# Optimization experiments

Measured on AMD Instinct MI355X. Metric: run time of the kernel, lower is better.

The kernel has to match this reference:

```python
import jax, jax.numpy as jnp
import numpy as np
import math

L = 6; D = 768; NH = 12; DH = D // NH; V = 2048; CTX = 512; B = 16; T = 512
PAD_ID = 0; PAD_X = 18; PAD_Y = 32; N_ACTIONS = 9


def _layernorm(x, s, b, eps=1e-5):
    m = jnp.mean(x, axis=-1, keepdims=True)
    v = jnp.mean((x - m) ** 2, axis=-1, keepdims=True)
    return (x - m) * jax.lax.rsqrt(v + eps) * s + b


def setup_inputs() -> dict:
    key = jax.random.key(0)
    ks = jax.random.split(key, 16)
    s = 0.02
    x_emb = jax.random.normal(ks[4], (19, D), jnp.float32) * s
    x_emb = x_emb.at[PAD_X].set(0.0)  # padding_idx row is zero in torch
    y_emb = jax.random.normal(ks[5], (33, D), jnp.float32) * s
    y_emb = y_emb.at[PAD_Y].set(0.0)
    return {
        "history_cards": jax.random.randint(ks[0], (B, T), 0, V),
        "history_players": jax.random.randint(ks[1], (B, T), 0, 2),
        "deck": jax.random.randint(ks[2], (B, 8), 0, V),
        "opp_deck": jax.random.randint(ks[3], (B, 8), 0, V),
        "tok_emb": jax.random.normal(ks[6], (V, D), jnp.float32) * s,
        "player_emb": jax.random.normal(ks[7], (2, D), jnp.float32) * s,
        "pos_emb": jax.random.normal(ks[8], (CTX, D), jnp.float32) * s,
        "x_emb": x_emb,
        "y_emb": y_emb,
        "ln1_s": jnp.ones((L, D), jnp.float32),
        "ln1_b": jnp.zeros((L, D), jnp.float32),
        "qkv_w": jax.random.normal(ks[9], (L, D, 3 * D), jnp.float32) * s,
        "qkv_b": jnp.zeros((L, 3 * D), jnp.float32),
        "proj_w": jax.random.normal(ks[10], (L, D, D), jnp.float32) * s,
        "proj_b": jnp.zeros((L, D), jnp.float32),
        "ln2_s": jnp.ones((L, D), jnp.float32),
        "ln2_b": jnp.zeros((L, D), jnp.float32),
        "fc1_w": jax.random.normal(ks[11], (L, D, 4 * D), jnp.float32) * s,
        "fc1_b": jnp.zeros((L, 4 * D), jnp.float32),
        "fc2_w": jax.random.normal(ks[12], (L, 4 * D, D), jnp.float32) * s,
        "fc2_b": jnp.zeros((L, D), jnp.float32),
        "lnf_s": jnp.ones((D,), jnp.float32),
        "lnf_b": jnp.zeros((D,), jnp.float32),
        "head_w": jax.random.normal(ks[13], (D, N_ACTIONS), jnp.float32) * s,
        "head_b": jnp.zeros((N_ACTIONS,), jnp.float32),
    }


def reference(history_cards, history_players, deck, opp_deck,
              tok_emb, player_emb, pos_emb, x_emb, y_emb,
              ln1_s, ln1_b, qkv_w, qkv_b, proj_w, proj_b,
              ln2_s, ln2_b, fc1_w, fc1_b, fc2_w, fc2_b,
              lnf_s, lnf_b, head_w, head_b):
    Bc, Tc = history_cards.shape
    attn_mask = history_cards != PAD_ID                      # (B,T) True = valid
    all_pad = ~jnp.any(attn_mask, axis=1)
    attn_mask = attn_mask.at[:, 0].set(attn_mask[:, 0] | all_pad)

    # multi-embedding sum (history_x/history_y are None => padding rows = 0)
    h = (tok_emb[history_cards]
         + player_emb[jnp.clip(history_players, 0, 1)]
         + x_emb[PAD_X] + y_emb[PAD_Y]
         + jnp.mean(tok_emb[deck], axis=1, keepdims=True)
         + jnp.mean(tok_emb[opp_deck], axis=1, keepdims=True))
    x = h + pos_emb[:Tc][None]                               # (B,T,D)

    causal = jnp.tril(jnp.ones((Tc, Tc), bool))
    mask = causal[None, None, :, :] & attn_mask[:, None, None, :]  # (B,1,T,T)
    neg_inf = jnp.float32(-jnp.inf)
    scale = 1.0 / math.sqrt(DH)

    for i in range(L):
        # attention
        xn = _layernorm(x, ln1_s[i], ln1_b[i])
        qkv = xn @ qkv_w[i] + qkv_b[i]
        q, k, v = jnp.split(qkv, 3, axis=-1)
        q = q.reshape(Bc, Tc, NH, DH)
        k = k.reshape(Bc, Tc, NH, DH)
        v = v.reshape(Bc, Tc, NH, DH)
        scores = jnp.einsum('bihd,bjhd->bhij', q, k) * scale
        scores = jnp.where(mask, scores, neg_inf)
        w = jax.nn.softmax(scores, axis=-1)
        w = jnp.nan_to_num(w, nan=0.0, posinf=0.0, neginf=0.0)
        y = jnp.einsum('bhij,bjhd->bihd', w, v).reshape(Bc, Tc, D)
        x = x + (y @ proj_w[i] + proj_b[i])
        # MLP
        xn = _layernorm(x, ln2_s[i], ln2_b[i])
        hmid = jax.nn.gelu(xn @ fc1_w[i] + fc1_b[i], approximate=False)
        x = x + (hmid @ fc2_w[i] + fc2_b[i])

    x = _layernorm(x, lnf_s, lnf_b)
    last_idx = jnp.clip(jnp.sum(attn_mask.astype(jnp.int32), axis=1) - 1, 0, None)
    last_h = x[jnp.arange(Bc), last_idx]                     # (B,D)
    return last_h @ head_w + head_b                          # (B,9)
```

## Files before the change

kernel.cpp:

```cpp
#include <hip/hip_runtime.h>
#include <hip/hip_bf16.h>
#include <math.h>

typedef __hip_bfloat16 bf16;
typedef __bf16 bf16x8 __attribute__((ext_vector_type(8)));
typedef float f32x4 __attribute__((ext_vector_type(4)));

__device__ __forceinline__ float b2f(bf16 v){ return __bfloat162float(v); }
__device__ __forceinline__ bf16  f2b(float v){ return __float2bfloat16(v); }

__device__ __forceinline__ float gelu_f(float v){
    float y = v * (1.f + 0.044715f * v * v);
    return v / (1.f + __expf(-1.5957691216057308f * y));
}

__device__ __forceinline__ void gl_lds16(const bf16* g, bf16* l) {
    __builtin_amdgcn_global_load_lds((const __attribute__((address_space(1))) unsigned int*)g,
                                     (__attribute__((address_space(3))) unsigned int*)l, 16, 0, 0);
}

__device__ __forceinline__ uint2 pack4bf(const float* v){
    union { unsigned short e[4]; uint2 u; } pk;
    #pragma unroll
    for (int r = 0; r < 4; r++) pk.e[r] = __builtin_bit_cast(unsigned short, f2b(v[r]));
    return pk.u;
}

__device__ __forceinline__ void phase_bar() {
    __builtin_amdgcn_sched_barrier(0);
    __builtin_amdgcn_s_barrier();
    __builtin_amdgcn_sched_barrier(0);
}

__global__ __launch_bounds__(256) void deckmean_k(const int* __restrict__ deck, const int* __restrict__ opp,
                                                  const float* __restrict__ tok, float* __restrict__ deckm)
{
    int b = blockIdx.x, w = blockIdx.y;
    const int* dk = (w ? opp : deck) + b * 8;
    int idx[8];
    #pragma unroll
    for (int j = 0; j < 8; j++) idx[j] = dk[j];
    float* out = deckm + (size_t)(w * 16 + b) * 768;
    for (int d = threadIdx.x; d < 768; d += 256) {
        float s = 0.f;
        #pragma unroll
        for (int j = 0; j < 8; j++) s += tok[(size_t)idx[j] * 768 + d];
        out[d] = s * 0.125f;
    }
}

__global__ __launch_bounds__(512) void mask_k(const int* __restrict__ cards, int* __restrict__ maskb,
                                              int* __restrict__ lastidx)
{
    int b = blockIdx.x, t = threadIdx.x;
    int m = (cards[b * 512 + t] != 0) ? 1 : 0;
    maskb[b * 512 + t] = m;
    __shared__ int red[512];
    red[t] = m; __syncthreads();
    for (int st = 256; st > 0; st >>= 1) { if (t < st) red[t] += red[t + st]; __syncthreads(); }
    if (t == 0) {
        int cnt = red[0];
        if (cnt == 0) { maskb[b * 512] = 1; cnt = 1; }
        lastidx[b] = cnt - 1;
    }
}

__global__ __launch_bounds__(256) void embed_k(const int* __restrict__ cards, const int* __restrict__ players,
                                               const float* __restrict__ tok, const float* __restrict__ pemb,
                                               const float* __restrict__ pos, const float* __restrict__ deckm,
                                               float* __restrict__ x)
{
    int t = blockIdx.x;
    int b = t >> 9, ti = t & 511;
    int cd = cards[t];
    int p = players[t]; p = p < 0 ? 0 : (p > 1 ? 1 : p);
    const float* tr  = tok  + (size_t)cd * 768;
    const float* pr  = pemb + (size_t)p  * 768;
    const float* po  = pos  + (size_t)ti * 768;
    const float* dm = deckm + (size_t)b * 768;
    const float* om = deckm + (size_t)(16 + b) * 768;
    float* xr = x + (size_t)t * 768;
    for (int d = threadIdx.x; d < 768; d += 256)
        xr[d] = tr[d] + pr[d] + po[d] + dm[d] + om[d];
}

__global__ __launch_bounds__(192) void ln_k(const float* __restrict__ x, const float* __restrict__ s,
                                            const float* __restrict__ b, bf16* __restrict__ out)
{
    int row = blockIdx.x, tid = threadIdx.x;
    float4 v = ((const float4*)(x + (size_t)row * 768))[tid];
    float sum = v.x + v.y + v.z + v.w;
    float sq  = v.x * v.x + v.y * v.y + v.z * v.z + v.w * v.w;
    #pragma unroll
    for (int off = 32; off > 0; off >>= 1) {
        sum += __shfl_xor(sum, off, 64);
        sq  += __shfl_xor(sq,  off, 64);
    }
    __shared__ float red[6];
    int wv = tid >> 6;
    if ((tid & 63) == 0) { red[wv] = sum; red[3 + wv] = sq; }
    __syncthreads();
    float S = red[0] + red[1] + red[2];
    float Q = red[3] + red[4] + red[5];
    float mean = S * (1.f / 768.f);
    float var  = Q * (1.f / 768.f) - mean * mean;
    float rstd = rsqrtf(var + 1e-5f);
    float4 sv = ((const float4*)s)[tid];
    float4 bv = ((const float4*)b)[tid];
    float o[4] = { (v.x - mean) * rstd * sv.x + bv.x, (v.y - mean) * rstd * sv.y + bv.y,
                   (v.z - mean) * rstd * sv.z + bv.z, (v.w - mean) * rstd * sv.w + bv.w };
    ((uint2*)(out + (size_t)row * 768))[tid] = pack4bf(o);
}

__global__ __launch_bounds__(256) void transpose4_k(const float* __restrict__ qw, const float* __restrict__ pw,
                                                    const float* __restrict__ f1, const float* __restrict__ f2,
                                                    bf16* __restrict__ oq, bf16* __restrict__ op,
                                                    bf16* __restrict__ o1, bf16* __restrict__ o2)
{
    int t = blockIdx.x;
    const float* in; bf16* out; int K, N, nbx;
    if (t < 432)       { in = qw; out = oq; K = 768;  N = 2304; nbx = 36; }
    else if (t < 576)  { in = pw; out = op; K = 768;  N = 768;  t -= 432;  nbx = 12; }
    else if (t < 1152) { in = f1; out = o1; K = 768;  N = 3072; t -= 576;  nbx = 48; }
    else               { in = f2; out = o2; K = 3072; N = 768;  t -= 1152; nbx = 12; }
    int n0 = (t % nbx) * 64, k0 = (t / nbx) * 64;
    int kq = threadIdx.x & 15, nq = threadIdx.x >> 4;
    float4 rr[4];
    #pragma unroll
    for (int r = 0; r < 4; r++)
        rr[r] = *(const float4*)&in[(size_t)(k0 + kq * 4 + r) * N + n0 + nq * 4];
    const float* fp = (const float*)rr;
    #pragma unroll
    for (int c = 0; c < 4; c++) {
        float v[4] = { fp[c], fp[4 + c], fp[8 + c], fp[12 + c] };
        *(uint2*)&out[(size_t)(n0 + nq * 4 + c) * K + k0 + kq * 4] = pack4bf(v);
    }
}

__global__ __launch_bounds__(512, 2) void gemm256_k(const bf16* __restrict__ A, const bf16* __restrict__ BT,
                                                    const float* __restrict__ bias, bf16* __restrict__ out,
                                                    int N, int K, int act, int nbn)
{
    __shared__ __align__(16) bf16 Asb[2][256 * 64];
    __shared__ __align__(16) bf16 Bsb[2][256 * 64];

    const int tid  = threadIdx.x;
    const int lane = tid & 63, wid = tid >> 6;
    const int quad = lane >> 4, l16 = lane & 15;
    const int wr = wid >> 2, wc = wid & 3;
    const int xr  = l16 & 7;
    const int cg0 = quad ^ xr;
    const int cg1 = cg0 ^ 4;

    const int nwg  = gridDim.x;
    const int wgid = ((int)blockIdx.x & 7) * (nwg >> 3) + ((int)blockIdx.x >> 3);
    const int mt = wgid / nbn, nt = wgid - mt * nbn;
    const int m0 = mt * 256, n0 = nt * 256;

    const int srow = wid * 8 + (lane >> 3);
    const int scg  = (lane & 7) ^ (lane >> 3);
    const bf16* sa[4]; const bf16* sb[4];
    #pragma unroll
    for (int s = 0; s < 4; s++) {
        sa[s] = A  + (size_t)(m0 + s * 64 + srow) * K + scg * 8;
        sb[s] = BT + (size_t)(n0 + s * 64 + srow) * K + scg * 8;
    }

#define STG_A(s, b) gl_lds16(sa[s], &Asb[b][((s) * 64 + wid * 8) * 64])
#define STG_B(s, b) gl_lds16(sb[s], &Bsb[b][((s) * 64 + wid * 8) * 64])
#define LD_B(cg) { _Pragma("unroll") for (int ni = 0; ni < 4; ni++) \
    bfv[ni] = __builtin_bit_cast(bf16x8, *(const uint4*)&Bc[(wc * 64 + ni * 16 + l16) * 64 + (cg) * 8]); }
#define LD_A(rb, cg) { _Pragma("unroll") for (int mi = 0; mi < 4; mi++) \
    afv[mi] = __builtin_bit_cast(bf16x8, *(const uint4*)&Ac[(wr * 128 + (rb) + mi * 16 + l16) * 64 + (cg) * 8]); }
#define MFMA16(MB) { _Pragma("unroll") for (int mi = 0; mi < 4; mi++) \
    _Pragma("unroll") for (int ni = 0; ni < 4; ni++) \
        acc[(MB) + mi][ni] = __builtin_amdgcn_mfma_f32_16x16x32_bf16(bfv[ni], afv[mi], acc[(MB) + mi][ni], 0, 0, 0); }

    STG_A(0, 0); STG_A(2, 0);
    STG_B(0, 0); STG_B(1, 0); STG_B(2, 0); STG_B(3, 0);
    STG_A(1, 0); STG_A(3, 0);
    #pragma unroll
    for (int s = 0; s < 4; s++) { sa[s] += 64; sb[s] += 64; }

    f32x4 acc[8][4] = {};

    asm volatile("s_waitcnt vmcnt(2)" ::: "memory");
    phase_bar();

    const int NKT = K >> 6;
    for (int kt = 0; kt < NKT; kt++) {
        const bf16* Ac = Asb[kt & 1];
        const bf16* Bc = Bsb[kt & 1];
        const int nxt = (kt & 1) ^ 1;
        const bool pf = (kt + 1 < NKT);
        bf16x8 bfv[4], afv[4];

        LD_B(cg0); LD_A(0, cg0);
        if (pf) {
            STG_A(0, nxt); STG_A(2, nxt);
            STG_B(0, nxt); STG_B(1, nxt); STG_B(2, nxt); STG_B(3, nxt);
            asm volatile("s_waitcnt vmcnt(6)" ::: "memory");
        } else {
            asm volatile("s_waitcnt vmcnt(0)" ::: "memory");
        }
        phase_bar();
        __builtin_amdgcn_s_setprio(1); MFMA16(0); __builtin_amdgcn_s_setprio(0);
        phase_bar();

        LD_A(64, cg0);
        if (pf) { STG_A(1, nxt); STG_A(3, nxt); }
        phase_bar();
        __builtin_amdgcn_s_setprio(1); MFMA16(4); __builtin_amdgcn_s_setprio(0);
        phase_bar();

        LD_B(cg1); LD_A(0, cg1);
        phase_bar();
        __builtin_amdgcn_s_setprio(1); MFMA16(0); __builtin_amdgcn_s_setprio(0);
        phase_bar();

        LD_A(64, cg1);
        phase_bar();
        __builtin_amdgcn_s_setprio(1); MFMA16(4); __builtin_amdgcn_s_setprio(0);
        asm volatile("s_waitcnt vmcnt(2)" ::: "memory");
        phase_bar();

        #pragma unroll
        for (int s = 0; s < 4; s++) { sa[s] += 64; sb[s] += 64; }
    }

    float4 bv[4];
    #pragma unroll
    for (int ni = 0; ni < 4; ni++)
        bv[ni] = *(const float4*)&bias[n0 + wc * 64 + ni * 16 + quad * 4];

    #pragma unroll
    for (int mi = 0; mi < 8; mi++) {
        const int m = m0 + wr * 128 + mi * 16 + l16;
        #pragma unroll
        for (int ni = 0; ni < 4; ni++) {
            const int nb2 = n0 + wc * 64 + ni * 16 + quad * 4;
            float v[4] = { acc[mi][ni][0] + bv[ni].x, acc[mi][ni][1] + bv[ni].y,
                           acc[mi][ni][2] + bv[ni].z, acc[mi][ni][3] + bv[ni].w };
            if (act) {
                #pragma unroll
                for (int r = 0; r < 4; r++) v[r] = gelu_f(v[r]);
            }
            *(uint2*)&out[(size_t)m * N + nb2] = pack4bf(v);
        }
    }
#undef STG_A
#undef STG_B
#undef LD_B
#undef LD_A
#undef MFMA16
}

__global__ __launch_bounds__(256) void gemm64_k(const bf16* __restrict__ A, const bf16* __restrict__ BT,
                                                const float* __restrict__ bias,
                                                float* __restrict__ x, int N, int K, int nb)
{
    __shared__ __align__(16) bf16 Al[64 * 64];
    __shared__ __align__(16) bf16 Bl[128 * 64];
    const int tid = threadIdx.x;
    const int lane = tid & 63, wave = tid >> 6;
    const int quad = lane >> 4, l16 = lane & 15;
    const int wm = wave >> 1, wn = wave & 1;

    const int bid = blockIdx.x;
    const int xcd = bid & 7, slot = bid >> 3;
    const int m_loc = slot / nb, nbl = slot - m_loc * nb;
    const int m0 = (xcd * 16 + m_loc) * 64, n0 = nbl * 128;

    f32x4 acc[2][4] = {};
    const int srow = wave * 8 + (lane >> 3);
    const int gcol = (lane & 7) * 8;

    for (int k0 = 0; k0 < K; k0 += 64) {
        #pragma unroll
        for (int i = 0; i < 2; i++)
            gl_lds16(&A [(size_t)(m0 + srow + i * 32) * K + k0 + gcol], &Al[(wave * 8 + i * 32) * 64]);
        #pragma unroll
        for (int i = 0; i < 4; i++)
            gl_lds16(&BT[(size_t)(n0 + srow + i * 32) * K + k0 + gcol], &Bl[(wave * 8 + i * 32) * 64]);
        __syncthreads();
        #pragma unroll
        for (int kk = 0; kk < 64; kk += 32) {
            bf16x8 af[2], bfr[4];
            #pragma unroll
            for (int t = 0; t < 2; t++)
                af[t]  = __builtin_bit_cast(bf16x8, *(const uint4*)(&Al[(wm * 32 + t * 16 + l16) * 64 + kk + quad * 8]));
            #pragma unroll
            for (int t = 0; t < 4; t++)
                bfr[t] = __builtin_bit_cast(bf16x8, *(const uint4*)(&Bl[(wn * 64 + t * 16 + l16) * 64 + kk + quad * 8]));
            #pragma unroll
            for (int tm = 0; tm < 2; tm++)
                #pragma unroll
                for (int tn = 0; tn < 4; tn++)
                    acc[tm][tn] = __builtin_amdgcn_mfma_f32_16x16x32_bf16(bfr[tn], af[tm], acc[tm][tn], 0, 0, 0);
        }
        __syncthreads();
    }

    float4 bv[4];
    #pragma unroll
    for (int tn = 0; tn < 4; tn++)
        bv[tn] = *(const float4*)&bias[n0 + wn * 64 + tn * 16 + quad * 4];

    #pragma unroll
    for (int tm = 0; tm < 2; tm++) {
        int m = m0 + wm * 32 + tm * 16 + l16;
        #pragma unroll
        for (int tn = 0; tn < 4; tn++) {
            int nbase = n0 + wn * 64 + tn * 16 + quad * 4;
            float* xp = &x[(size_t)m * N + nbase];
            float4 xo = *(float4*)xp;
            xo.x += acc[tm][tn][0] + bv[tn].x;
            xo.y += acc[tm][tn][1] + bv[tn].y;
            xo.z += acc[tm][tn][2] + bv[tn].z;
            xo.w += acc[tm][tn][3] + bv[tn].w;
            *(float4*)xp = xo;
        }
    }
}

__global__ __launch_bounds__(256) void attn_k(const bf16* __restrict__ qkv, const int* __restrict__ mask,
                                              bf16* __restrict__ y)
{
    const int qt = blockIdx.x, h = blockIdx.y, b = blockIdx.z;
    const int qbase = qt * 128, tokb = b * 512;
    __shared__ __align__(16) unsigned short Kl[128][72];
    __shared__ __align__(16) unsigned short Vt[64][136];
    __shared__ __align__(16) unsigned short Ptq[4][16][136];
    __shared__ float mkf[128];

    const int tid = threadIdx.x, wave = tid >> 6, lane = tid & 63;
    const int quad = lane >> 4, l16 = lane & 15;

    bf16x8 bq[2][2];
    #pragma unroll
    for (int qc = 0; qc < 2; qc++) {
        const bf16* qp = &qkv[(size_t)(tokb + qbase + wave * 32 + qc * 16 + l16) * 2304 + h * 64];
        bq[qc][0] = __builtin_bit_cast(bf16x8, *(const uint4*)(qp + quad * 8));
        bq[qc][1] = __builtin_bit_cast(bf16x8, *(const uint4*)(qp + 32 + quad * 8));
    }

    float m_i[2] = { -INFINITY, -INFINITY }, l_i[2] = { 0.f, 0.f };
    f32x4 Oacc[2][4] = {};

    const int nst = qt + 1;
    for (int s = 0; s < nst; s++) {
        const int j0 = s * 128;
        __syncthreads();
        {
            int key = tid >> 1, c0 = (tid & 1) * 32;
            const bf16* kg = &qkv[(size_t)(tokb + j0 + key) * 2304 + 768  + h * 64 + c0];
            const bf16* vg = &qkv[(size_t)(tokb + j0 + key) * 2304 + 1536 + h * 64 + c0];
            #pragma unroll
            for (int q = 0; q < 4; q++)
                *(uint4*)&Kl[key][c0 + q * 8] = *(const uint4*)(kg + q * 8);
            union { uint4 u[4]; unsigned short e[32]; } vv;
            #pragma unroll
            for (int q = 0; q < 4; q++) vv.u[q] = *(const uint4*)(vg + q * 8);
            #pragma unroll
            for (int j = 0; j < 32; j++) Vt[c0 + j][key] = vv.e[j];
            if (tid < 128) mkf[tid] = mask[b * 512 + j0 + tid] ? 0.f : -INFINITY;
        }
        __syncthreads();

        #pragma unroll
        for (int qc = 0; qc < 2; qc++) {
            const int qi = qbase + wave * 32 + qc * 16 + l16;

            f32x4 sc[8] = {};
            #pragma unroll
            for (int kcc = 0; kcc < 8; kcc++) {
                bf16x8 af0 = __builtin_bit_cast(bf16x8, *(const uint4*)&Kl[kcc * 16 + l16][quad * 8]);
                bf16x8 af1 = __builtin_bit_cast(bf16x8, *(const uint4*)&Kl[kcc * 16 + l16][32 + quad * 8]);
                sc[kcc] = __builtin_amdgcn_mfma_f32_16x16x32_bf16(af0, bq[qc][0], sc[kcc], 0, 0, 0);
                sc[kcc] = __builtin_amdgcn_mfma_f32_16x16x32_bf16(af1, bq[qc][1], sc[kcc], 0, 0, 0);
            }

            float pv[8][4];
            float mx = -INFINITY;
            #pragma unroll
            for (int kcc = 0; kcc < 8; kcc++) {
                float4 mk4 = *(const float4*)&mkf[kcc * 16 + quad * 4];
                float mkr[4] = { mk4.x, mk4.y, mk4.z, mk4.w };
                #pragma unroll
                for (int r = 0; r < 4; r++) {
                    int krel = kcc * 16 + quad * 4 + r;
                    float sval = (j0 + krel <= qi) ? (sc[kcc][r] * 0.125f + mkr[r]) : -INFINITY;
                    pv[kcc][r] = sval;
                    mx = fmaxf(mx, sval);
                }
            }
            mx = fmaxf(mx, __shfl_xor(mx, 16, 64));
            mx = fmaxf(mx, __shfl_xor(mx, 32, 64));
            float mn = fmaxf(m_i[qc], mx);
            float alpha = (mn == -INFINITY) ? 1.f : __expf(m_i[qc] - mn);
            float lsum = 0.f;
            #pragma unroll
            for (int kcc = 0; kcc < 8; kcc++)
                #pragma unroll
                for (int r = 0; r < 4; r++) {
                    float pp = (pv[kcc][r] == -INFINITY) ? 0.f : __expf(pv[kcc][r] - mn);
                    pv[kcc][r] = pp; lsum += pp;
                }
            lsum += __shfl_xor(lsum, 16, 64);
            lsum += __shfl_xor(lsum, 32, 64);
            m_i[qc] = mn; l_i[qc] = alpha * l_i[qc] + lsum;

            #pragma unroll
            for (int kcc = 0; kcc < 8; kcc++)
                *(uint2*)&Ptq[wave][l16][kcc * 16 + quad * 4] = pack4bf(pv[kcc]);
            #pragma unroll
            for (int mc = 0; mc < 4; mc++)
                #pragma unroll
                for (int r = 0; r < 4; r++) Oacc[qc][mc][r] *= alpha;

            __syncthreads();

            #pragma unroll
            for (int kcc = 0; kcc < 4; kcc++) {
                bf16x8 pb = __builtin_bit_cast(bf16x8, *(const uint4*)&Ptq[wave][l16][kcc * 32 + quad * 8]);
                #pragma unroll
                for (int mc = 0; mc < 4; mc++) {
                    bf16x8 vf = __builtin_bit_cast(bf16x8, *(const uint4*)&Vt[mc * 16 + l16][kcc * 32 + quad * 8]);
                    Oacc[qc][mc] = __builtin_amdgcn_mfma_f32_16x16x32_bf16(vf, pb, Oacc[qc][mc], 0, 0, 0);
                }
            }
        }
    }

    #pragma unroll
    for (int qc = 0; qc < 2; qc++) {
        float inv = (l_i[qc] > 0.f) ? 1.f / l_i[qc] : 0.f;
        const int tok = tokb + qbase + wave * 32 + qc * 16 + l16;
        #pragma unroll
        for (int mc = 0; mc < 4; mc++) {
            float v[4] = { Oacc[qc][mc][0] * inv, Oacc[qc][mc][1] * inv,
                           Oacc[qc][mc][2] * inv, Oacc[qc][mc][3] * inv };
            *(uint2*)&y[(size_t)tok * 768 + h * 64 + mc * 16 + quad * 4] = pack4bf(v);
        }
    }
}

__global__ __launch_bounds__(256) void head_k(const float* __restrict__ x, const int* __restrict__ lastidx,
                                              const float* __restrict__ ls, const float* __restrict__ lb,
                                              const float* __restrict__ hw, const float* __restrict__ hb,
                                              float* __restrict__ out)
{
    int b = blockIdx.x, tid = threadIdx.x;
    const float* xr = x + ((size_t)(b * 512 + lastidx[b])) * 768;
    float v0 = xr[tid], v1 = xr[tid + 256], v2 = xr[tid + 512];
    __shared__ float rs[256], rq[256];
    rs[tid] = v0 + v1 + v2; rq[tid] = v0 * v0 + v1 * v1 + v2 * v2;
    __syncthreads();
    for (int st = 128; st > 0; st >>= 1) {
        if (tid < st) { rs[tid] += rs[tid + st]; rq[tid] += rq[tid + st]; }
        __syncthreads();
    }
    float mean = rs[0] * (1.f / 768.f);
    float var  = rq[0] * (1.f / 768.f) - mean * mean;
    float rstd = rsqrtf(var + 1e-5f);
    float part[9];
    #pragma unroll
    for (int a = 0; a < 9; a++) part[a] = 0.f;
    float vv[3] = { v0, v1, v2 };
    #pragma unroll
    for (int e = 0; e < 3; e++) {
        int d = tid + e * 256;
        float xnv = (vv[e] - mean) * rstd * ls[d] + lb[d];
        #pragma unroll
        for (int a = 0; a < 9; a++) part[a] += xnv * hw[d * 9 + a];
    }
    __shared__ float r9[9][256];
    #pragma unroll
    for (int a = 0; a < 9; a++) r9[a][tid] = part[a];
    __syncthreads();
    for (int st = 128; st > 0; st >>= 1) {
        if (tid < st) {
            for (int a = 0; a < 9; a++) r9[a][tid] += r9[a][tid + st];
        }
        __syncthreads();
    }
    if (tid < 9) out[b * 9 + tid] = r9[tid][0] + hb[tid];
}

extern "C" void kernel_launch(void* const* d_in, const int* in_sizes, int n_in,
                              void* d_out, int out_size, void* d_ws, size_t ws_size,
                              hipStream_t stream) {
    const int*   cards   = (const int*)  d_in[0];
    const int*   players = (const int*)  d_in[1];
    const int*   deck    = (const int*)  d_in[2];
    const int*   oppd    = (const int*)  d_in[3];
    const float* tok     = (const float*)d_in[4];
    const float* pemb    = (const float*)d_in[5];
    const float* pos     = (const float*)d_in[6];
    const float* ln1s  = (const float*)d_in[9];
    const float* ln1b  = (const float*)d_in[10];
    const float* qkvw  = (const float*)d_in[11];
    const float* qkvb  = (const float*)d_in[12];
    const float* projw = (const float*)d_in[13];
    const float* projb = (const float*)d_in[14];
    const float* ln2s  = (const float*)d_in[15];
    const float* ln2b  = (const float*)d_in[16];
    const float* fc1w  = (const float*)d_in[17];
    const float* fc1b  = (const float*)d_in[18];
    const float* fc2w  = (const float*)d_in[19];
    const float* fc2b  = (const float*)d_in[20];
    const float* lnfs  = (const float*)d_in[21];
    const float* lnfb  = (const float*)d_in[22];
    const float* hw    = (const float*)d_in[23];
    const float* hb    = (const float*)d_in[24];
    float* out = (float*)d_out;

    char* p = (char*)d_ws;
    auto alloc = [&](size_t bytes) { char* q = p; p += (bytes + 255) & ~((size_t)255); return q; };
    float* x     = (float*)alloc(8192ull * 768 * 4);
    bf16*  xn    = (bf16*) alloc(8192ull * 768 * 2);
    bf16*  big   = (bf16*) alloc(8192ull * 3072 * 2);
    bf16*  wt    = (bf16*) alloc(7077888ull * 2);
    float* deckm = (float*)alloc(2ull * 16 * 768 * 4);
    int*   maskb = (int*)  alloc(8192ull * 4);
    int*   lasti = (int*)  alloc(64);

    bf16* wq = wt;
    bf16* wp = wq + 2304ull * 768;
    bf16* w1 = wp + 768ull * 768;
    bf16* w2 = w1 + 3072ull * 768;

    deckmean_k<<<dim3(16, 2), 256, 0, stream>>>(deck, oppd, tok, deckm);
    mask_k<<<16, 512, 0, stream>>>(cards, maskb, lasti);
    embed_k<<<8192, 256, 0, stream>>>(cards, players, tok, pemb, pos, deckm, x);

    for (int i = 0; i < 6; i++) {
        transpose4_k<<<1728, 256, 0, stream>>>(
            qkvw + (size_t)i * 768 * 2304, projw + (size_t)i * 768 * 768,
            fc1w + (size_t)i * 768 * 3072, fc2w + (size_t)i * 3072 * 768,
            wq, wp, w1, w2);

        ln_k<<<8192, 192, 0, stream>>>(x, ln1s + i * 768, ln1b + i * 768, xn);
        gemm256_k<<<288, 512, 0, stream>>>(xn, wq, qkvb + i * 2304, big, 2304, 768, 0, 9);
        attn_k<<<dim3(4, 12, 16), 256, 0, stream>>>(big, maskb, xn);
        gemm64_k<<<128 * 6, 256, 0, stream>>>(xn, wp, projb + i * 768, x, 768, 768, 6);
        ln_k<<<8192, 192, 0, stream>>>(x, ln2s + i * 768, ln2b + i * 768, xn);
        gemm256_k<<<384, 512, 0, stream>>>(xn, w1, fc1b + i * 3072, big, 3072, 768, 1, 12);
        gemm64_k<<<128 * 6, 256, 0, stream>>>(big, w2, fc2b + i * 768, x, 768, 3072, 6);
    }

    head_k<<<16, 256, 0, stream>>>(x, lasti, lnfs, lnfb, hw, hb, out);
}
```

Baseline: 1.997 ms.

## Replace residual GEMM with 256x128-tile triple-buffered pipelined kernel

Swaps the simple 64x128 single-buffered residual-add GEMM used for the attention projection and fc2 for a 256x128 tile kernel with 512 threads. The new kernel keeps three LDS stages filled by direct global-to-LDS loads, uses an XOR-swizzled layout, and raises wave priority around the MFMA blocks. The aim is to overlap memory loads with matrix math and get more reuse per tile. The trade-off is a grid of only 192 workgroups, which may leave some compute units idle, plus a much larger LDS footprint per block.

Result: no change. 1.971 ms (-1.3%).

```diff
diff --git a/kernel.cpp b/kernel.cpp
--- a/kernel.cpp
+++ b/kernel.cpp
@@ -255,72 +255,102 @@
 #undef MFMA16
 }
 
-__global__ __launch_bounds__(256) void gemm64_k(const bf16* __restrict__ A, const bf16* __restrict__ BT,
-                                                const float* __restrict__ bias,
-                                                float* __restrict__ x, int N, int K, int nb)
-{
-    __shared__ __align__(16) bf16 Al[64 * 64];
-    __shared__ __align__(16) bf16 Bl[128 * 64];
-    const int tid = threadIdx.x;
-    const int lane = tid & 63, wave = tid >> 6;
+__global__ __launch_bounds__(512, 2) void gemmn128_k(const bf16* __restrict__ A, const bf16* __restrict__ BT,
+                                                     const float* __restrict__ bias, float* __restrict__ x,
+                                                     int N, int K, int nbn)
+{
+    __shared__ __align__(16) bf16 Asb[3][256 * 64];
+    __shared__ __align__(16) bf16 Bsb[3][128 * 64];
+
+    const int tid  = threadIdx.x;
+    const int lane = tid & 63, wid = tid >> 6;
     const int quad = lane >> 4, l16 = lane & 15;
-    const int wm = wave >> 1, wn = wave & 1;
-
-    const int bid = blockIdx.x;
-    const int xcd = bid & 7, slot = bid >> 3;
-    const int m_loc = slot / nb, nbl = slot - m_loc * nb;
-    const int m0 = (xcd * 16 + m_loc) * 64, n0 = nbl * 128;
-
-    f32x4 acc[2][4] = {};
-    const int srow = wave * 8 + (lane >> 3);
-    const int gcol = (lane & 7) * 8;
-
-    for (int k0 = 0; k0 < K; k0 += 64) {
-        #pragma unroll
-        for (int i = 0; i < 2; i++)
-            gl_lds16(&A [(size_t)(m0 + srow + i * 32) * K + k0 + gcol], &Al[(wave * 8 + i * 32) * 64]);
-        #pragma unroll
-        for (int i = 0; i < 4; i++)
-            gl_lds16(&BT[(size_t)(n0 + srow + i * 32) * K + k0 + gcol], &Bl[(wave * 8 + i * 32) * 64]);
-        __syncthreads();
-        #pragma unroll
-        for (int kk = 0; kk < 64; kk += 32) {
-            bf16x8 af[2], bfr[4];
-            #pragma unroll
-            for (int t = 0; t < 2; t++)
-                af[t]  = __builtin_bit_cast(bf16x8, *(const uint4*)(&Al[(wm * 32 + t * 16 + l16) * 64 + kk + quad * 8]));
-            #pragma unroll
-            for (int t = 0; t < 4; t++)
-                bfr[t] = __builtin_bit_cast(bf16x8, *(const uint4*)(&Bl[(wn * 64 + t * 16 + l16) * 64 + kk + quad * 8]));
-            #pragma unroll
-            for (int tm = 0; tm < 2; tm++)
-                #pragma unroll
-                for (int tn = 0; tn < 4; tn++)
-                    acc[tm][tn] = __builtin_amdgcn_mfma_f32_16x16x32_bf16(bfr[tn], af[tm], acc[tm][tn], 0, 0, 0);
-        }
-        __syncthreads();
-    }
-
-    float4 bv[4];
-    #pragma unroll
-    for (int tn = 0; tn < 4; tn++)
-        bv[tn] = *(const float4*)&bias[n0 + wn * 64 + tn * 16 + quad * 4];
-
-    #pragma unroll
-    for (int tm = 0; tm < 2; tm++) {
-        int m = m0 + wm * 32 + tm * 16 + l16;
-        #pragma unroll
-        for (int tn = 0; tn < 4; tn++) {
-            int nbase = n0 + wn * 64 + tn * 16 + quad * 4;
-            float* xp = &x[(size_t)m * N + nbase];
+    const int wr = wid >> 1, wc = wid & 1;
+    const int cg0 = quad ^ (l16 & 7);
+    const int cg1 = cg0 ^ 4;
+
+    const int nwg  = gridDim.x;
+    const int wgid = ((int)blockIdx.x & 7) * (nwg >> 3) + ((int)blockIdx.x >> 3);
+    const int mt = wgid / nbn, nt = wgid - mt * nbn;
+    const int m0 = mt * 256, n0 = nt * 128;
+
+    const int srow = wid * 8 + (lane >> 3);
+    const int scg  = (lane & 7) ^ (lane >> 3);
+    const bf16* sa[4]; const bf16* sb[2];
+    #pragma unroll
+    for (int s = 0; s < 4; s++) sa[s] = A  + (size_t)(m0 + s * 64 + srow) * K + scg * 8;
+    #pragma unroll
+    for (int s = 0; s < 2; s++) sb[s] = BT + (size_t)(n0 + s * 64 + srow) * K + scg * 8;
+
+#define NSTG_A(s, b) gl_lds16(sa[s], &Asb[b][((s) * 64 + wid * 8) * 64])
+#define NSTG_B(s, b) gl_lds16(sb[s], &Bsb[b][((s) * 64 + wid * 8) * 64])
+#define NSTG6(b) { NSTG_A(0, b); NSTG_A(1, b); NSTG_A(2, b); NSTG_A(3, b); NSTG_B(0, b); NSTG_B(1, b); }
+#define NADV { _Pragma("unroll") for (int s = 0; s < 4; s++) sa[s] += 64; sb[0] += 64; sb[1] += 64; }
+#define NLD(cg, b) { _Pragma("unroll") for (int i = 0; i < 4; i++) { \
+    bfv[i] = __builtin_bit_cast(bf16x8, *(const uint4*)&Bsb[b][(wc * 64 + i * 16 + l16) * 64 + (cg) * 8]); \
+    afv[i] = __builtin_bit_cast(bf16x8, *(const uint4*)&Asb[b][(wr * 64 + i * 16 + l16) * 64 + (cg) * 8]); } }
+#define NMFMA { _Pragma("unroll") for (int mi = 0; mi < 4; mi++) \
+    _Pragma("unroll") for (int ni = 0; ni < 4; ni++) \
+        acc[mi][ni] = __builtin_amdgcn_mfma_f32_16x16x32_bf16(bfv[ni], afv[mi], acc[mi][ni], 0, 0, 0); }
+#define NITER(CUR, ST) { \
+    const bool pf = (kt + 2 < NKT); \
+    NLD(cg0, CUR); \
+    if (pf) { NSTG6(ST); NADV; } \
+    phase_bar(); \
+    __builtin_amdgcn_s_setprio(1); NMFMA; __builtin_amdgcn_s_setprio(0); \
+    phase_bar(); \
+    NLD(cg1, CUR); \
+    phase_bar(); \
+    __builtin_amdgcn_s_setprio(1); NMFMA; __builtin_amdgcn_s_setprio(0); \
+    if (pf)               { asm volatile("s_waitcnt vmcnt(6)" ::: "memory"); phase_bar(); } \
+    else if (kt + 1 < NKT){ asm volatile("s_waitcnt vmcnt(0)" ::: "memory"); phase_bar(); } \
+    kt++; \
+}
+
+    f32x4 acc[4][4] = {};
+    const int NKT = K >> 6;
+
+    NSTG6(0); NADV;
+    NSTG6(1); NADV;
+    asm volatile("s_waitcnt vmcnt(6)" ::: "memory");
+    phase_bar();
+
+    int kt = 0;
+    bf16x8 bfv[4], afv[4];
+    #pragma unroll 1
+    for (int kt3 = 0; kt3 < NKT; kt3 += 3) {
+        NITER(0, 2);
+        NITER(1, 0);
+        NITER(2, 1);
+    }
+
+    float4 bv4[4];
+    #pragma unroll
+    for (int ni = 0; ni < 4; ni++)
+        bv4[ni] = *(const float4*)&bias[n0 + wc * 64 + ni * 16 + quad * 4];
+
+    #pragma unroll
+    for (int mi = 0; mi < 4; mi++) {
+        const int m = m0 + wr * 64 + mi * 16 + l16;
+        #pragma unroll
+        for (int ni = 0; ni < 4; ni++) {
+            const int nb2 = n0 + wc * 64 + ni * 16 + quad * 4;
+            float* xp = &x[(size_t)m * N + nb2];
             float4 xo = *(float4*)xp;
-            xo.x += acc[tm][tn][0] + bv[tn].x;
-            xo.y += acc[tm][tn][1] + bv[tn].y;
-            xo.z += acc[tm][tn][2] + bv[tn].z;
-            xo.w += acc[tm][tn][3] + bv[tn].w;
+            xo.x += acc[mi][ni][0] + bv4[ni].x;
+            xo.y += acc[mi][ni][1] + bv4[ni].y;
+            xo.z += acc[mi][ni][2] + bv4[ni].z;
+            xo.w += acc[mi][ni][3] + bv4[ni].w;
             *(float4*)xp = xo;
         }
     }
+#undef NSTG_A
+#undef NSTG_B
+#undef NSTG6
+#undef NADV
+#undef NLD
+#undef NMFMA
+#undef NITER
 }
 
 __global__ __launch_bounds__(256) void attn_k(const bf16* __restrict__ qkv, const int* __restrict__ mask,
@@ -543,10 +573,10 @@
         ln_k<<<8192, 192, 0, stream>>>(x, ln1s + i * 768, ln1b + i * 768, xn);
         gemm256_k<<<288, 512, 0, stream>>>(xn, wq, qkvb + i * 2304, big, 2304, 768, 0, 9);
         attn_k<<<dim3(4, 12, 16), 256, 0, stream>>>(big, maskb, xn);
-        gemm64_k<<<128 * 6, 256, 0, stream>>>(xn, wp, projb + i * 768, x, 768, 768, 6);
+        gemmn128_k<<<192, 512, 0, stream>>>(xn, wp, projb + i * 768, x, 768, 768, 6);
         ln_k<<<8192, 192, 0, stream>>>(x, ln2s + i * 768, ln2b + i * 768, xn);
         gemm256_k<<<384, 512, 0, stream>>>(xn, w1, fc1b + i * 3072, big, 3072, 768, 1, 12);
-        gemm64_k<<<128 * 6, 256, 0, stream>>>(big, w2, fc2b + i * 768, x, 768, 3072, 6);
+        gemmn128_k<<<192, 512, 0, stream>>>(big, w2, fc2b + i * 768, x, 768, 3072, 6);
     }
 
     head_k<<<16, 256, 0, stream>>>(x, lasti, lnfs, lnfb, hw, hb, out);
```
